# Kernel tuning notes

Hardware: AMD Instinct MI355X
Metric: run time of the kernel (lower is better)

Reference implementation:

```python
import jax, jax.numpy as jnp
import numpy as np


def setup_inputs() -> dict:
    key = jax.random.key(0)
    k1, k2, k3, k4 = jax.random.split(key, 4)
    N, C, H, W = 1, 512, 192, 192
    F, K = 512, 3
    x = jax.random.normal(k1, (N, C, H, W), dtype=jnp.float32)
    w = jax.random.normal(k2, (F, C, K, K), dtype=jnp.float32) * 0.05
    b = jax.random.normal(k3, (F,), dtype=jnp.float32)
    # binary RoI mask over output spatial grid (stands in for PIL polygon raster)
    mask = jax.random.randint(k4, (H, W), 0, 2, dtype=jnp.int32)
    return {"x": x, "w": w, "b": b, "mask": mask}


def reference(x, w, b, mask):
    # my_conv: im2col conv (stride=1, pad=1), gather rows where mask==1,
    # GEMM, scatter back into zeros, then add bias everywhere (res += b
    # happens AFTER the scatter). Equivalent dense form: conv(x,w)*mask + b.
    conv = jax.lax.conv_general_dilated(
        x, w,
        window_strides=(1, 1),
        padding=((1, 1), (1, 1)),
        dimension_numbers=("NCHW", "OIHW", "NCHW"),
    )  # [N, F, H, W]
    m = mask.astype(conv.dtype)[None, None, :, :]
    return conv * m + b[None, :, None, None]
```

## Files before the change

kernel.cpp:

```cpp
#include <hip/hip_runtime.h>


typedef unsigned short ushort_t;
typedef __attribute__((ext_vector_type(8))) __bf16 bf16x8;
typedef __attribute__((ext_vector_type(4))) float f32x4;
typedef __attribute__((ext_vector_type(8))) unsigned short ushort8;

#define IMG_W 192
#define IMG_H 192
#define HW    36864
#define PAD_W 194
#define C_IN  512
#define F_OUT 512
#define KTOT  4608
#define NCBLK 144

__device__ __forceinline__ unsigned short f2bf(float f) {
  unsigned int u = __builtin_bit_cast(unsigned int, f);
  u += 0x7fffu + ((u >> 16) & 1u);
  return (unsigned short)(u >> 16);
}

__device__ __forceinline__ void async16(const void* g, void* l) {
  __builtin_amdgcn_global_load_lds(
      (const __attribute__((address_space(1))) unsigned int*)g,
      (__attribute__((address_space(3))) unsigned int*)l, 16, 0, 0);
}

__global__ void prep_all(const float* __restrict__ x, const float* __restrict__ w,
                         const float* __restrict__ bias,
                         ushort_t* __restrict__ Xt, ushort_t* __restrict__ Wt,
                         int* __restrict__ counter, float* __restrict__ out) {
  __shared__ float tile[64][65];
  const int bid = blockIdx.x;
  const int tid = threadIdx.x;

  if (bid < 4608) {
    const int p  = bid;
    const int w0 = (p % 3) * 64;
    const int c0 = ((p / 3) & 7) * 64;
    const int h  = p / 24;

    const int wl_r = tid & 63;
    const int cg_r = tid >> 6;
    const float* src = x + (size_t)(c0 + cg_r * 16) * HW + (size_t)h * IMG_W + w0 + wl_r;
#pragma unroll
    for (int cc = 0; cc < 16; ++cc)
      tile[cg_r * 16 + cc][wl_r] = src[(size_t)cc * HW];
    __syncthreads();

    const int wl = tid >> 2;
    const int cg = tid & 3;
    ushort_t* dst = Xt + ((size_t)(h + 1) * PAD_W + (w0 + wl + 1)) * C_IN + c0 + cg * 16;
    ushort8 v0, v1;
#pragma unroll
    for (int cc = 0; cc < 8; ++cc) v0[cc] = f2bf(tile[cg * 16 + cc][wl]);
#pragma unroll
    for (int cc = 0; cc < 8; ++cc) v1[cc] = f2bf(tile[cg * 16 + 8 + cc][wl]);
    *(ushort8*)dst = v0;
    *(ushort8*)(dst + 8) = v1;
  } else if (bid < 4801) {
    const int idx = (bid - 4608) * 256 + tid;
    const int p   = idx >> 6;
    const int off = (idx & 63) * 8;
    int r, c;
    if (p < 388) { r = (p >= 194) ? 193 : 0; c = (p >= 194) ? p - 194 : p; }
    else         { int q = p - 388; r = 1 + (q >> 1); c = (q & 1) ? 193 : 0; }
    ushort8 z = {0, 0, 0, 0, 0, 0, 0, 0};
    *(ushort8*)(Xt + ((size_t)r * PAD_W + c) * C_IN + off) = z;
  } else if (bid < 5825) {
    const int idx = (bid - 4801) * 256 + tid;
    const int f = idx >> 9;
    const int c = idx & 511;
    const float* src = w + (size_t)idx * 9;
    float v[9];
#pragma unroll
    for (int t = 0; t < 9; ++t) v[t] = src[t];
    ushort_t* dst = Wt + (size_t)f * KTOT + c;
#pragma unroll
    for (int t = 0; t < 9; ++t) dst[t * C_IN] = f2bf(v[t]);
  } else if (bid == 5825) {
  } else {
    const int g = (bid - 5826) * 256 + tid;
    f32x4* o4 = (f32x4*)out;
#pragma unroll
    for (int it = 0; it < 9; ++it) {
      const int n4 = g + it * 524288;
      const int f  = n4 / (HW / 4);
      const float bv = bias[f];
      f32x4 v = {bv, bv, bv, bv};
      o4[n4] = v;
    }
  }
}

__global__ void compact_count(const int* __restrict__ mask,
                              int* __restrict__ counts) {
  __shared__ int wcnt[4];
  const int i = blockIdx.x * 256 + threadIdx.x;
  const int lane = threadIdx.x & 63;
  const int wave = threadIdx.x >> 6;
  unsigned long long b = __ballot(mask[i] != 0);
  if (lane == 0) wcnt[wave] = __popcll(b);
  __syncthreads();
  if (threadIdx.x == 0)
    counts[blockIdx.x] = wcnt[0] + wcnt[1] + wcnt[2] + wcnt[3];
}

__global__ void compact_scatter(const int* __restrict__ mask,
                                const int* __restrict__ counts,
                                int* __restrict__ list, int* __restrict__ counter) {
  __shared__ int woff[4];
  const int bid  = blockIdx.x;
  const int tid  = threadIdx.x;
  const int lane = tid & 63;
  const int wave = tid >> 6;
  const int i = bid * 256 + tid;
  const int m = mask[i];
  unsigned long long b = __ballot(m != 0);
  if (lane == 0) woff[wave] = __popcll(b);
  __syncthreads();
  if (tid == 0) {
    int acc = 0;
    for (int k = 0; k < bid; ++k) acc += counts[k];
    const int c0 = woff[0], c1 = woff[1], c2 = woff[2], c3 = woff[3];
    woff[0] = acc; woff[1] = acc + c0; woff[2] = acc + c0 + c1;
    woff[3] = acc + c0 + c1 + c2;
    if (bid == NCBLK - 1) counter[0] = acc + c0 + c1 + c2 + c3;
  }
  __syncthreads();
  if (m) list[woff[wave] + __popcll(b & ((1ull << lane) - 1ull))] = i;
}

__global__ __launch_bounds__(256, 3) void conv_gemm(
    const ushort_t* __restrict__ Wt, const ushort_t* __restrict__ Xt,
    const float* __restrict__ bias, const int* __restrict__ list,
    const int* __restrict__ counter, float* __restrict__ out) {
  __shared__ __align__(16) ushort_t As[128 * 64];
  __shared__ __align__(16) ushort_t Bs[128 * 64];

  const int count = counter[0];
  const int n0 = blockIdx.x * 128;
  if (n0 >= count) return;

  const int tid  = threadIdx.x;
  const int lane = tid & 63;
  const int wave = tid >> 6;
  const int wm   = wave >> 1;
  const int wn   = wave & 1;
  const int m0   = blockIdx.y * 128;

  const int rrel = lane >> 3;
  const int q    = (lane & 7) ^ rrel;

  const ushort_t* aSrc = Wt + (size_t)(m0 + wave * 32 + rrel) * KTOT + q * 8;

  unsigned int bOffs[4];
#pragma unroll
  for (int ii = 0; ii < 4; ++ii) {
    const int pos = n0 + wave * 32 + ii * 8 + rrel;
    const int pix = (pos < count) ? list[pos] : 0;
    const int hh = pix / IMG_W, ww = pix - hh * IMG_W;
    bOffs[ii] = ((hh + 1) * PAD_W + (ww + 1)) * C_IN + q * 8;
  }

  ushort_t* aDst = &As[wave * 32 * 64];
  ushort_t* bDst = &Bs[wave * 32 * 64];

  const int col  = lane & 15;
  const int quad = lane >> 4;

  f32x4 acc[4][4] = {};

  {
    const int toff0 = -(PAD_W + 1) * C_IN;
#pragma unroll
    for (int ii = 0; ii < 4; ++ii) {
      async16(aSrc + (size_t)ii * 8 * KTOT, aDst + ii * 512);
      async16(Xt + (int)bOffs[ii] + toff0, bDst + ii * 512);
    }
  }

#pragma unroll 1
  for (int kk = 0; kk < 72; ++kk) {
    __syncthreads();
    bf16x8 af[2][4], bfr[2][4];
#pragma unroll
    for (int s = 0; s < 2; ++s) {
#pragma unroll
      for (int i = 0; i < 4; ++i) {
        const int row = wm * 64 + i * 16 + col;
        af[s][i] = *(const bf16x8*)&As[row * 64 + ((s * 4 + quad) ^ (row & 7)) * 8];
      }
#pragma unroll
      for (int j = 0; j < 4; ++j) {
        const int row = wn * 64 + j * 16 + col;
        bfr[s][j] = *(const bf16x8*)&Bs[row * 64 + ((s * 4 + quad) ^ (row & 7)) * 8];
      }
    }
    if (kk < 71) {
      __syncthreads();
      const int kn   = kk + 1;
      const int tapn = kn >> 3;
      const int kcn  = (kn & 7) * 64;
      const int toffn = ((tapn / 3) * PAD_W + (tapn % 3) - (PAD_W + 1)) * C_IN;
      const int aoffn = tapn * 512 + kcn;
#pragma unroll
      for (int ii = 0; ii < 4; ++ii) {
        async16(aSrc + (size_t)ii * 8 * KTOT + aoffn, aDst + ii * 512);
        async16(Xt + (int)bOffs[ii] + toffn + kcn, bDst + ii * 512);
      }
    }
#pragma unroll
    for (int s = 0; s < 2; ++s)
#pragma unroll
      for (int i = 0; i < 4; ++i)
#pragma unroll
        for (int j = 0; j < 4; ++j)
          acc[i][j] = __builtin_amdgcn_mfma_f32_16x16x32_bf16(af[s][i], bfr[s][j],
                                                              acc[i][j], 0, 0, 0);
  }

#pragma unroll
  for (int j = 0; j < 4; ++j) {
    const int pos = n0 + wn * 64 + j * 16 + col;
    if (pos < count) {
      const int n_pix = list[pos];
#pragma unroll
      for (int i = 0; i < 4; ++i) {
        const int mrow = m0 + wm * 64 + i * 16 + quad * 4;
        float* o = out + (size_t)mrow * HW + n_pix;
#pragma unroll
        for (int r = 0; r < 4; ++r)
          o[(size_t)r * HW] = acc[i][j][r] + bias[mrow + r];
      }
    }
  }
}

extern "C" void kernel_launch(void* const* d_in, const int* in_sizes, int n_in,
                              void* d_out, int out_size, void* d_ws, size_t ws_size,
                              hipStream_t stream) {
  const float* x    = (const float*)d_in[0];
  const float* w    = (const float*)d_in[1];
  const float* bias = (const float*)d_in[2];
  const int*   mask = (const int*)d_in[3];
  float* out = (float*)d_out;

  int* list    = (int*)d_ws;
  int* counter = list + HW;
  int* counts  = counter + 1;
  ushort_t* Xt = (ushort_t*)((char*)d_ws + 148096);
  ushort_t* Wt = Xt + (size_t)PAD_W * PAD_W * C_IN;

  prep_all<<<dim3(7874), 256, 0, stream>>>(x, w, bias, Xt, Wt, counter, out);
  compact_count<<<dim3(NCBLK), 256, 0, stream>>>(mask, counts);
  compact_scatter<<<dim3(NCBLK), 256, 0, stream>>>(mask, counts, list, counter);
  conv_gemm<<<dim3((HW + 127) / 128, F_OUT / 128), 256, 0, stream>>>(
      Wt, Xt, bias, list, counter, out);
}
```

Measured before the change: 265.2 us.

## Fold bias fill into conv GEMM mainloop and merge mask count into prep

Result: no change. 263.0 us (-0.8%).

```diff
diff --git a/kernel.cpp b/kernel.cpp
--- a/kernel.cpp
+++ b/kernel.cpp
@@ -28,10 +28,11 @@
 }
 
 __global__ void prep_all(const float* __restrict__ x, const float* __restrict__ w,
-                         const float* __restrict__ bias,
+                         const int* __restrict__ mask,
                          ushort_t* __restrict__ Xt, ushort_t* __restrict__ Wt,
-                         int* __restrict__ counter, float* __restrict__ out) {
+                         int* __restrict__ counts) {
   __shared__ float tile[64][65];
+  __shared__ int wcnt[4];
   const int bid = blockIdx.x;
   const int tid = threadIdx.x;
 
@@ -79,32 +80,16 @@
     ushort_t* dst = Wt + (size_t)f * KTOT + c;
 #pragma unroll
     for (int t = 0; t < 9; ++t) dst[t * C_IN] = f2bf(v[t]);
-  } else if (bid == 5825) {
   } else {
-    const int g = (bid - 5826) * 256 + tid;
-    f32x4* o4 = (f32x4*)out;
-#pragma unroll
-    for (int it = 0; it < 9; ++it) {
-      const int n4 = g + it * 524288;
-      const int f  = n4 / (HW / 4);
-      const float bv = bias[f];
-      f32x4 v = {bv, bv, bv, bv};
-      o4[n4] = v;
-    }
-  }
-}
-
-__global__ void compact_count(const int* __restrict__ mask,
-                              int* __restrict__ counts) {
-  __shared__ int wcnt[4];
-  const int i = blockIdx.x * 256 + threadIdx.x;
-  const int lane = threadIdx.x & 63;
-  const int wave = threadIdx.x >> 6;
-  unsigned long long b = __ballot(mask[i] != 0);
-  if (lane == 0) wcnt[wave] = __popcll(b);
-  __syncthreads();
-  if (threadIdx.x == 0)
-    counts[blockIdx.x] = wcnt[0] + wcnt[1] + wcnt[2] + wcnt[3];
+    const int cbid = bid - 5825;
+    const int i = cbid * 256 + tid;
+    const int lane = tid & 63;
+    const int wave = tid >> 6;
+    unsigned long long b = __ballot(mask[i] != 0);
+    if (lane == 0) wcnt[wave] = __popcll(b);
+    __syncthreads();
+    if (tid == 0) counts[cbid] = wcnt[0] + wcnt[1] + wcnt[2] + wcnt[3];
+  }
 }
 
 __global__ void compact_scatter(const int* __restrict__ mask,
@@ -141,14 +126,30 @@
 
   const int count = counter[0];
   const int n0 = blockIdx.x * 128;
-  if (n0 >= count) return;
-
+  const int m0 = blockIdx.y * 128;
   const int tid  = threadIdx.x;
+
+  int lo_pix, hi_pix;
+  {
+    const int loPos = n0, hiPos = n0 + 128;
+    lo_pix = (loPos == 0) ? 0 : ((loPos <= count) ? list[loPos - 1] + 1 : HW);
+    hi_pix = (hiPos <= count) ? list[hiPos - 1] + 1 : HW;
+    if (hi_pix < lo_pix) hi_pix = lo_pix;
+  }
+
+  if (n0 >= count) {
+    for (int rr = 0; rr < 128; ++rr) {
+      const float bv = bias[m0 + rr];
+      float* o = out + (size_t)(m0 + rr) * HW;
+      for (int p = lo_pix + tid; p < hi_pix; p += 256) o[p] = bv;
+    }
+    return;
+  }
+
   const int lane = tid & 63;
   const int wave = tid >> 6;
   const int wm   = wave >> 1;
   const int wn   = wave & 1;
-  const int m0   = blockIdx.y * 128;
 
   const int rrel = lane >> 3;
   const int q    = (lane & 7) ^ rrel;
@@ -209,6 +210,15 @@
       for (int ii = 0; ii < 4; ++ii) {
         async16(aSrc + (size_t)ii * 8 * KTOT + aoffn, aDst + ii * 512);
         async16(Xt + (int)bOffs[ii] + toffn + kcn, bDst + ii * 512);
+      }
+    }
+    if (kk < 64) {
+#pragma unroll
+      for (int rr2 = 0; rr2 < 2; ++rr2) {
+        const int rr = kk * 2 + rr2;
+        const float bv = bias[m0 + rr];
+        float* o = out + (size_t)(m0 + rr) * HW;
+        for (int p = lo_pix + tid; p < hi_pix; p += 256) o[p] = bv;
       }
     }
 #pragma unroll
@@ -253,8 +263,7 @@
   ushort_t* Xt = (ushort_t*)((char*)d_ws + 148096);
   ushort_t* Wt = Xt + (size_t)PAD_W * PAD_W * C_IN;
 
-  prep_all<<<dim3(7874), 256, 0, stream>>>(x, w, bias, Xt, Wt, counter, out);
-  compact_count<<<dim3(NCBLK), 256, 0, stream>>>(mask, counts);
+  prep_all<<<dim3(5969), 256, 0, stream>>>(x, w, mask, Xt, Wt, counts);
   compact_scatter<<<dim3(NCBLK), 256, 0, stream>>>(mask, counts, list, counter);
   conv_gemm<<<dim3((HW + 127) / 128, F_OUT / 128), 256, 0, stream>>>(
       Wt, Xt, bias, list, counter, out);
```
